# Kernel tuning notes

Hardware: AMD Instinct MI355X
Metric: run time of the kernel (lower is better)

## Reference

```python
import jax, jax.numpy as jnp
import numpy as np

N = 512
E = 64          # neigh_dim = spatial_dim + vel_dim
HID = 256
OUT = 32
SPAT = 32
VEL = 32

_OFFDIAG = np.flatnonzero(~np.eye(N, dtype=bool))  # static off-diagonal flat indices


def setup_inputs() -> dict:
    key = jax.random.key(0)
    ks = jax.random.split(key, 24)
    g = lambda i, shape, s=0.05: jax.random.normal(ks[i], shape, dtype=jnp.float32) * s
    return {
        "hidden_state": jax.random.normal(ks[0], (N, HID), dtype=jnp.float32),
        "obs1": jax.random.normal(ks[1], (N, 2), dtype=jnp.float32),
        "obs2": jax.random.normal(ks[2], (N, 2), dtype=jnp.float32),
        "h0": g(3, (N, N, E), 0.1),
        "c0": g(4, (N, N, E), 0.1),
        "W_s": g(5, (SPAT, 2)), "b_s": g(6, (SPAT,)),
        "W_v": g(7, (VEL, 2)), "b_v": g(8, (VEL,)),
        "W_hs": g(9, (E, HID)), "b_hs": g(10, (E,)),
        "W_ih": g(11, (4 * E, E)), "b_ih": g(12, (4 * E,)),
        "W_hh": g(13, (4 * E, E)), "b_hh": g(14, (4 * E,)),
        "Wq": g(15, (E, E)), "Wk": g(16, (E, E)), "Wv": g(17, (E, E)),
        "W_in": g(18, (3 * E, E)), "b_in": g(19, (3 * E,)),
        "W_out": g(20, (E, E)), "b_out": g(21, (E,)),
        "W_o": g(22, (OUT, E)), "b_o": g(23, (OUT,)),
        "track_mask": jnp.ones((N,), dtype=bool),
    }


def _forward(hidden_state, obs1, obs2, h0, c0, W_s, b_s, W_v, b_v, W_hs, b_hs,
             W_ih, b_ih, W_hh, b_hh, Wq, Wk, Wv, W_in, b_in, W_out, b_out, W_o, b_o):
    # pairwise relative positions / velocities, off-diagonal only: [N*(N-1), 2]
    rel_pos = (obs2[None, :, :] - obs2[:, None, :]).reshape(N * N, 2)[_OFFDIAG]
    vel = obs2 - obs1
    rel_vel = (vel[None, :, :] - vel[:, None, :]).reshape(N * N, 2)[_OFFDIAG]

    spat_embed = jax.nn.relu(rel_pos @ W_s.T + b_s)
    vel_embed = jax.nn.relu((rel_vel * 4.0) @ W_v.T + b_v)
    rel_embed = jnp.concatenate([spat_embed, vel_embed], axis=1)  # [M, E]

    # gather off-diagonal LSTM states and run one LSTMCell step
    h = h0.reshape(N * N, E)[_OFFDIAG]
    c = c0.reshape(N * N, E)[_OFFDIAG]
    gates = rel_embed @ W_ih.T + b_ih + h @ W_hh.T + b_hh  # [M, 4E]
    i_g, f_g, g_g, o_g = jnp.split(gates, 4, axis=1)
    c_new = jax.nn.sigmoid(f_g) * c + jax.nn.sigmoid(i_g) * jnp.tanh(g_g)
    h_new = jax.nn.sigmoid(o_g) * jnp.tanh(c_new)  # [M, E]

    hs = hidden_state @ W_hs.T + b_hs  # [N, E]
    # embedded: [N, N, E] -> transpose to (L=N, B=N, E)
    embedded = jnp.concatenate([hs[:, None, :], h_new.reshape(N, N - 1, E)], axis=1)
    embedded = jnp.transpose(embedded, (1, 0, 2))

    q = embedded @ Wq.T
    k = embedded @ Wk.T
    v = embedded @ Wv.T

    # torch MultiheadAttention (1 head) internal projections
    Wq2, Wk2, Wv2 = jnp.split(W_in, 3, axis=0)
    bq2, bk2, bv2 = jnp.split(b_in, 3, axis=0)
    scale = 1.0 / jnp.sqrt(jnp.float32(E))
    q2 = (q @ Wq2.T + bq2) * scale
    k2 = k @ Wk2.T + bk2
    v2 = v @ Wv2.T + bv2
    scores = jnp.einsum('lbe,sbe->bls', q2, k2)      # [B=N, L=N, S=N]
    attn = jax.nn.softmax(scores, axis=-1)
    ctx = jnp.einsum('bls,sbe->lbe', attn, v2)       # [L, B, E]
    attn_out = ctx @ W_out.T + b_out

    attn_vectors = attn_out[0]                        # [N, E]
    return attn_vectors @ W_o.T + b_o                 # [N, OUT]


def reference(hidden_state, obs1, obs2, h0, c0, W_s, b_s, W_v, b_v, W_hs, b_hs,
              W_ih, b_ih, W_hh, b_hh, Wq, Wk, Wv, W_in, b_in, W_out, b_out,
              W_o, b_o, track_mask):
    # track_mask assumed all-True: adj_matrix == off-diagonal mask.
    return _forward(hidden_state, obs1, obs2, h0, c0, W_s, b_s, W_v, b_v,
                    W_hs, b_hs, W_ih, b_ih, W_hh, b_hh, Wq, Wk, Wv,
                    W_in, b_in, W_out, b_out, W_o, b_o)
```

## Files before the change

kernel.cpp:

```cpp
#include <hip/hip_runtime.h>
#include <cstdint>

#define NN 512
#define EE 64
#define HIDD 256
#define OUTD 32
#define L2E 1.4426950408889634f

typedef __bf16 bf16x8 __attribute__((ext_vector_type(8)));
typedef __bf16 bf16x4 __attribute__((ext_vector_type(4)));
typedef float f32x4 __attribute__((ext_vector_type(4)));
typedef float f32x2 __attribute__((ext_vector_type(2)));

__device__ float g_WhsT[HIDD*EE];
__device__ uint4 g_Ag2[4096];
__device__ float g_biasI[256];
__device__ float g_embW[EE*4];
__device__ float g_WqT[EE*EE];
__device__ float g_Wq2T[EE*EE];
__device__ float g_WvT[EE*EE];
__device__ float g_Wv2T[EE*EE];
__device__ float g_WoutT[EE*EE];
__device__ float g_WoT[EE*OUTD];

__device__ __forceinline__ float ex2(float x){ return __builtin_amdgcn_exp2f(x); }
__device__ __forceinline__ float rcp_(float x){ return __builtin_amdgcn_rcpf(x); }

__global__ __launch_bounds__(256) void prepW(
    const float* __restrict__ W_ih, const float* __restrict__ b_ih,
    const float* __restrict__ W_hh, const float* __restrict__ b_hh,
    const float* __restrict__ Wq, const float* __restrict__ Wv,
    const float* __restrict__ W_in, const float* __restrict__ W_hs,
    const float* __restrict__ W_s, const float* __restrict__ b_s,
    const float* __restrict__ W_v, const float* __restrict__ b_v,
    const float* __restrict__ W_out, const float* __restrict__ W_o)
{
    const int blk = blockIdx.x, tid = threadIdx.x;
    if (blk < 8) {
#pragma unroll
        for (int ii = 0; ii < 2; ++ii) {
            int idx = blk*512 + ii*256 + tid;
            int w = idx >> 9, mh = (idx >> 8) & 1, kh = (idx >> 6) & 3, lane = idx & 63;
            int m = lane & 15, qq = m >> 2, gate = m & 3;
            int e = 8*w + 2*qq + mh;
            int o = gate*64 + e;
            int kb = kh*32 + (lane >> 4)*8;
            float sc = (gate == 2) ? (-2.f*L2E) : (-L2E);
            bf16x8 vv;
#pragma unroll
            for (int j = 0; j < 8; ++j) {
                int k = kb + j;
                float raw = (k < 64) ? W_ih[o*64 + k] : W_hh[o*64 + (k - 64)];
                vv[j] = (__bf16)(sc * raw);
            }
            g_Ag2[idx] = __builtin_bit_cast(uint4, vv);
        }
    } else if (blk == 8) {
        {
            int e = tid >> 2, gate = tid & 3, o = gate*64 + e;
            float sc = (gate == 2) ? (-2.f*L2E) : (-L2E);
            g_biasI[tid] = sc * (b_ih[o] + b_hh[o]);
        }
        if (tid < 64) {
            int e = tid;
            if (e < 32) {
                g_embW[e*4+0] = W_s[e*2]; g_embW[e*4+1] = W_s[e*2+1]; g_embW[e*4+2] = b_s[e];
            } else {
                g_embW[e*4+0] = 4.f*W_v[(e-32)*2]; g_embW[e*4+1] = 4.f*W_v[(e-32)*2+1]; g_embW[e*4+2] = b_v[e-32];
            }
            g_embW[e*4+3] = 0.f;
        }
    } else if (blk == 9) {
        __shared__ float T[64][65];
        for (int kt = 0; kt < 4; ++kt) {
            __syncthreads();
#pragma unroll
            for (int i = 0; i < 16; ++i) {
                int row = i*4 + (tid >> 6);
                int col = tid & 63;
                T[col][row] = W_hs[row*256 + kt*64 + col];
            }
            __syncthreads();
#pragma unroll
            for (int i = 0; i < 16; ++i) {
                int krow = i*4 + (tid >> 6);
                int e = tid & 63;
                g_WhsT[(kt*64 + krow)*64 + e] = T[krow][e];
            }
        }
    } else {
        __shared__ float T[64][65];
        auto tr64 = [&](const float* src, float* dst) {
#pragma unroll
            for (int i = 0; i < 16; ++i) {
                int row = i*4 + (tid >> 6), col = tid & 63;
                T[col][row] = src[row*64 + col];
            }
            __syncthreads();
#pragma unroll
            for (int i = 0; i < 16; ++i) {
                int k = i*4 + (tid >> 6), e = tid & 63;
                dst[k*64 + e] = T[k][e];
            }
            __syncthreads();
        };
        if (blk == 10) {
            tr64(Wq, g_WqT);
            tr64(W_in, g_Wq2T);
        } else if (blk == 11) {
            tr64(Wv, g_WvT);
            tr64(W_in + 2*4096, g_Wv2T);
        } else {
            tr64(W_out, g_WoutT);
#pragma unroll
            for (int i = 0; i < 8; ++i) {
                int row = i*4 + (tid >> 6), col = tid & 63;
                T[col][row] = W_o[row*64 + col];
            }
            __syncthreads();
#pragma unroll
            for (int i = 0; i < 8; ++i) {
                int k = i*8 + (tid >> 5), o = tid & 31;
                g_WoT[k*32 + o] = T[k][o];
            }
        }
    }
}

__global__ __launch_bounds__(512, 4) void row_kernel(
    const float* __restrict__ hidden, const float* __restrict__ b_hs,
    const float* __restrict__ obs1, const float* __restrict__ obs2,
    const float* __restrict__ h0, const float* __restrict__ c0,
    const float* __restrict__ W_in, const float* __restrict__ Wk,
    const float* __restrict__ b_in, const float* __restrict__ b_out,
    const float* __restrict__ b_o, float* __restrict__ out)
{
    __shared__ __align__(16) float Hs[3][32*64];
    __shared__ __align__(16) float Cs[3][32*64];
    __shared__ __align__(16) unsigned short Xe[2][32*64];
    __shared__ float spart[2][8][32];
    __shared__ float2 obs1L[NN], obs2L[NN];
    __shared__ float hid[HIDD];
    __shared__ float part[8][64];
    __shared__ float hsL[64], qkL[64];
    __shared__ float vA[64], vB[64];
    __shared__ float ctxE[64];

    const int b = blockIdx.x, tid = threadIdx.x;
    const int w = tid >> 6, l = tid & 63;
    const int q = l >> 4, r = l & 15;
    const int ebase0 = 8*w + 2*q;
    const float* h0r = h0 + (size_t)b*NN*EE;
    const float* c0r = c0 + (size_t)b*NN*EE;

    auto stageT = [&](const float* gsrc, float* lbuf) {
        const int row = tid >> 4;
        const int cb  = (tid & 15) * 16;
        const char* g = (const char*)gsrc + row*256 + (cb ^ ((row & 15) << 4));
        char* lp = (char*)lbuf + tid*16;
        __builtin_amdgcn_global_load_lds(
            (const __attribute__((address_space(1))) void*)g,
            (__attribute__((address_space(3))) void*)lp, 16, 0, 0);
    };

    auto matvecG = [&](const float* M, const float* vin, float* vout,
                       const float* bias, float scale) {
        float s = 0.f;
#pragma unroll
        for (int k2 = 0; k2 < 8; ++k2) {
            int kk = w*8 + k2;
            s = fmaf(M[kk*64 + l], vin[kk], s);
        }
        part[w][l] = s;
        asm volatile("s_waitcnt lgkmcnt(0)" ::: "memory");
        __builtin_amdgcn_s_barrier();
        if (tid < 64) {
            float v = bias ? bias[tid] : 0.f;
#pragma unroll
            for (int i = 0; i < 8; ++i) v += part[i][tid];
            vout[tid] = v * scale;
        }
        asm volatile("s_waitcnt lgkmcnt(0)" ::: "memory");
        __builtin_amdgcn_s_barrier();
    };

    uint4 Afr[2][4];
#pragma unroll
    for (int mh = 0; mh < 2; ++mh)
#pragma unroll
        for (int kh = 0; kh < 4; ++kh)
            Afr[mh][kh] = g_Ag2[w*512 + mh*256 + kh*64 + l];
    f32x4 biasv[2];
#pragma unroll
    for (int mh = 0; mh < 2; ++mh) {
        float4 t4 = *(const float4*)(g_biasI + (ebase0 + mh)*4);
        biasv[mh][0]=t4.x; biasv[mh][1]=t4.y; biasv[mh][2]=t4.z; biasv[mh][3]=t4.w;
    }
    float eA[4], eB[4], eC[4];
    {
        const int e0 = (tid & 15)*4;
#pragma unroll
        for (int i = 0; i < 4; ++i) {
            eA[i] = g_embW[(e0+i)*4+0]; eB[i] = g_embW[(e0+i)*4+1]; eC[i] = g_embW[(e0+i)*4+2];
        }
    }

    const float ob2x = obs2[b*2], ob2y = obs2[b*2+1];
    const float ob1x = obs1[b*2], ob1y = obs1[b*2+1];
    const float velbx = ob2x - ob1x, velby = ob2y - ob1y;
    auto embedW = [&](int jb, unsigned short* xe) {
        const int p = tid >> 4;
        const float2 o2 = obs2L[jb + p];
        const float2 o1 = obs1L[jb + p];
        const float u0s = o2.x - ob2x, u1s = o2.y - ob2y;
        const float u0v = (o2.x - o1.x) - velbx, u1v = (o2.y - o1.y) - velby;
        const bool sph = ((tid & 15) < 8);
        const float u0 = sph ? u0s : u0v, u1 = sph ? u1s : u1v;
        bf16x4 pk;
#pragma unroll
        for (int i = 0; i < 4; ++i)
            pk[i] = (__bf16)fmaxf(fmaf(eA[i], u0, fmaf(eB[i], u1, eC[i])), 0.f);
        *(bf16x4*)((char*)xe + p*128 + (((tid & 15)*8) ^ ((p & 7) << 4))) = pk;
    };

    stageT(h0r, Hs[0]);
    stageT(c0r, Cs[0]);
    stageT(h0r + 32*EE, Hs[1]);
    stageT(c0r + 32*EE, Cs[1]);
    obs2L[tid] = ((const float2*)obs2)[tid];
    obs1L[tid] = ((const float2*)obs1)[tid];
    if (tid < HIDD) hid[tid] = hidden[b*HIDD + tid];
    asm volatile("s_waitcnt lgkmcnt(0)" ::: "memory");
    __builtin_amdgcn_s_barrier();
    __builtin_amdgcn_sched_barrier(0);
    {
        float s = 0.f;
#pragma unroll 8
        for (int k2 = 0; k2 < 32; ++k2) {
            int kk = w*32 + k2;
            s = fmaf(g_WhsT[kk*64 + l], hid[kk], s);
        }
        part[w][l] = s;
    }
    asm volatile("s_waitcnt lgkmcnt(0)" ::: "memory");
    __builtin_amdgcn_s_barrier();
    if (tid < 64) {
        float v = b_hs[tid];
#pragma unroll
        for (int i = 0; i < 8; ++i) v += part[i][tid];
        hsL[tid] = v;
    }
    asm volatile("s_waitcnt lgkmcnt(0)" ::: "memory");
    __builtin_amdgcn_s_barrier();
    matvecG(g_WqT,       hsL, vA, nullptr, 1.f);
    matvecG(g_Wq2T,      vA,  vB, b_in,    1.f);
    matvecG(W_in + 4096, vB,  vA, nullptr, 1.f);
    matvecG(Wk,          vA,  qkL, nullptr, L2E*0.125f);
    embedW(0, Xe[0]);
    const f32x2 qkr = *(const f32x2*)&qkL[ebase0];
    const f32x2 hsd = *(const f32x2*)&hsL[ebase0];
    asm volatile("s_waitcnt vmcnt(2) lgkmcnt(0)" ::: "memory");
    __builtin_amdgcn_s_barrier();
    __builtin_amdgcn_sched_barrier(0);

    float m_run = -__builtin_inff(), l_run = 0.f;
    float ctxa[2] = {0.f, 0.f};
    float Eev[2][2];
    int hb = 0;

#pragma unroll 1
    for (int t = 0; t < 16; ++t) {
        const int base = t*32;
        const int cx = t & 1;

        if (t > 0) {
            const int c = l & 31;
            const float* spp = &spart[cx ^ 1][0][0];
            float s_p = spp[c];
#pragma unroll
            for (int i = 1; i < 8; ++i) s_p += spp[i*32 + c];
            float tm = s_p;
#pragma unroll
            for (int off = 1; off < 32; off <<= 1) tm = fmaxf(tm, __shfl_xor(tm, off, 64));
            float m_new = fmaxf(m_run, tm);
            float corr = ex2(m_run - m_new);
            float wp = ex2(s_p - m_new);
            l_run = fmaf(l_run, corr, wp);
            m_run = m_new;
            float wn0 = __shfl(wp, r, 64);
            float wn1 = __shfl(wp, 16 + r, 64);
#pragma unroll
            for (int mh = 0; mh < 2; ++mh)
                ctxa[mh] = fmaf(wn1, Eev[mh][1], fmaf(wn0, Eev[mh][0], ctxa[mh]*corr));
        }

        const float* HsC = &Hs[hb][0];
        const float* CsC = &Cs[hb][0];
        const unsigned short* XeC = &Xe[cx][0];
        f32x2 cpre[2];
#pragma unroll
        for (int nh = 0; nh < 2; ++nh) {
            const int p = 16*nh + r;
            cpre[nh] = *(const f32x2*)((const char*)CsC + p*256 +
                        ((ebase0*4) ^ ((p & 15) << 4)));
        }
        f32x4 acc[2][2];
#pragma unroll
        for (int mh = 0; mh < 2; ++mh)
#pragma unroll
            for (int nh = 0; nh < 2; ++nh) acc[mh][nh] = biasv[mh];
#pragma unroll
        for (int kh = 0; kh < 4; ++kh) {
            const bf16x8 Af0 = __builtin_bit_cast(bf16x8, Afr[0][kh]);
            const bf16x8 Af1 = __builtin_bit_cast(bf16x8, Afr[1][kh]);
#pragma unroll
            for (int nh = 0; nh < 2; ++nh) {
                const int p = 16*nh + r;
                bf16x8 Bf;
                if (kh < 2) {
                    Bf = *(const bf16x8*)((const char*)XeC + p*128 +
                          ((kh*64 + q*16) ^ ((p & 7) << 4)));
                } else {
                    const char* hbp = (const char*)HsC + p*256;
                    const int cbb = (kh - 2)*128 + q*32;
                    const int sw = (p & 15) << 4;
                    f32x4 f0 = *(const f32x4*)(hbp + (cbb ^ sw));
                    f32x4 f1 = *(const f32x4*)(hbp + ((cbb + 16) ^ sw));
                    Bf[0]=(__bf16)f0[0]; Bf[1]=(__bf16)f0[1]; Bf[2]=(__bf16)f0[2]; Bf[3]=(__bf16)f0[3];
                    Bf[4]=(__bf16)f1[0]; Bf[5]=(__bf16)f1[1]; Bf[6]=(__bf16)f1[2]; Bf[7]=(__bf16)f1[3];
                }
                acc[0][nh] = __builtin_amdgcn_mfma_f32_16x16x32_bf16(Af0, Bf, acc[0][nh], 0, 0, 0);
                acc[1][nh] = __builtin_amdgcn_mfma_f32_16x16x32_bf16(Af1, Bf, acc[1][nh], 0, 0, 0);
            }
        }
        float sp[2] = {0.f, 0.f};
#pragma unroll
        for (int nh = 0; nh < 2; ++nh) {
#pragma unroll
            for (int mh = 0; mh < 2; ++mh) {
                f32x4 g4 = acc[mh][nh];
                float ea = ex2(g4[0]);
                float eg = ex2(g4[2]);
                float itg = (1.f - eg) * rcp_((1.f + ea)*(1.f + eg));
                float sf = rcp_(1.f + ex2(g4[1]));
                float cn = fmaf(sf, cpre[nh][mh], itg);
                float eo = ex2(g4[3]);
                float ec = ex2(-2.f*L2E*cn);
                float h = (1.f - ec) * rcp_((1.f + eo)*(1.f + ec));
                h = (16*nh + r == b - base) ? hsd[mh] : h;
                Eev[mh][nh] = h;
                sp[nh] = fmaf(qkr[mh], h, sp[nh]);
            }
        }
#pragma unroll
        for (int nh = 0; nh < 2; ++nh) {
            float v = sp[nh];
            v += __shfl_xor(v, 16, 64);
            v += __shfl_xor(v, 32, 64);
            if (q == 0) spart[cx][w][16*nh + r] = v;
        }

        if (t < 14) {
            const int hb2 = (hb == 0) ? 2 : hb - 1;
            stageT(h0r + (size_t)(t+2)*32*EE, &Hs[hb2][0]);
            stageT(c0r + (size_t)(t+2)*32*EE, &Cs[hb2][0]);
        }
        if (t < 15) embedW(base + 32, &Xe[cx ^ 1][0]);

        if (t < 14) {
            asm volatile("s_waitcnt vmcnt(2) lgkmcnt(0)" ::: "memory");
        } else {
            asm volatile("s_waitcnt vmcnt(0) lgkmcnt(0)" ::: "memory");
        }
        __builtin_amdgcn_s_barrier();
        __builtin_amdgcn_sched_barrier(0);
        hb = (hb == 2) ? 0 : hb + 1;
    }

    {
        const int c = l & 31;
        const float* spp = &spart[1][0][0];
        float s_p = spp[c];
#pragma unroll
        for (int i = 1; i < 8; ++i) s_p += spp[i*32 + c];
        float tm = s_p;
#pragma unroll
        for (int off = 1; off < 32; off <<= 1) tm = fmaxf(tm, __shfl_xor(tm, off, 64));
        float m_new = fmaxf(m_run, tm);
        float corr = ex2(m_run - m_new);
        float wp = ex2(s_p - m_new);
        l_run = fmaf(l_run, corr, wp);
        m_run = m_new;
        float wn0 = __shfl(wp, r, 64);
        float wn1 = __shfl(wp, 16 + r, 64);
#pragma unroll
        for (int mh = 0; mh < 2; ++mh)
            ctxa[mh] = fmaf(wn1, Eev[mh][1], fmaf(wn0, Eev[mh][0], ctxa[mh]*corr));
    }

    float lred = l_run;
    lred += __shfl_xor(lred, 1, 64); lred += __shfl_xor(lred, 2, 64);
    lred += __shfl_xor(lred, 4, 64); lred += __shfl_xor(lred, 8, 64);
    lred += __shfl_xor(lred, 16, 64);
    const float inv = rcp_(lred);
#pragma unroll
    for (int mh = 0; mh < 2; ++mh) {
        float v = ctxa[mh];
        v += __shfl_xor(v, 1, 64); v += __shfl_xor(v, 2, 64);
        v += __shfl_xor(v, 4, 64); v += __shfl_xor(v, 8, 64);
        if (r == 0) ctxE[ebase0 + mh] = v * inv;
    }
    __syncthreads();
    matvecG(g_WvT,   ctxE, vA, nullptr,    1.f);
    matvecG(g_Wv2T,  vA,   vB, b_in + 128, 1.f);
    matvecG(g_WoutT, vB,   vA, b_out,      1.f);
    {
        if (l < 32) {
            float s = 0.f;
#pragma unroll
            for (int k2 = 0; k2 < 8; ++k2) {
                int kk = w*8 + k2;
                s = fmaf(g_WoT[kk*32 + l], vA[kk], s);
            }
            part[w][l] = s;
        }
        __syncthreads();
        if (tid < 32) {
            float v = b_o[tid];
#pragma unroll
            for (int i = 0; i < 8; ++i) v += part[i][tid];
            out[b*OUTD + tid] = v;
        }
    }
}

extern "C" void kernel_launch(void* const* d_in, const int* in_sizes, int n_in,
                              void* d_out, int out_size, void* d_ws, size_t ws_size,
                              hipStream_t stream) {
    const float* hidden = (const float*)d_in[0];
    const float* obs1   = (const float*)d_in[1];
    const float* obs2   = (const float*)d_in[2];
    const float* h0     = (const float*)d_in[3];
    const float* c0     = (const float*)d_in[4];
    const float* W_s    = (const float*)d_in[5];
    const float* b_s    = (const float*)d_in[6];
    const float* W_v    = (const float*)d_in[7];
    const float* b_v    = (const float*)d_in[8];
    const float* W_hs   = (const float*)d_in[9];
    const float* b_hs   = (const float*)d_in[10];
    const float* W_ih   = (const float*)d_in[11];
    const float* b_ih   = (const float*)d_in[12];
    const float* W_hh   = (const float*)d_in[13];
    const float* b_hh   = (const float*)d_in[14];
    const float* Wq     = (const float*)d_in[15];
    const float* Wk     = (const float*)d_in[16];
    const float* Wv     = (const float*)d_in[17];
    const float* W_in   = (const float*)d_in[18];
    const float* b_in   = (const float*)d_in[19];
    const float* W_out  = (const float*)d_in[20];
    const float* b_out  = (const float*)d_in[21];
    const float* W_o    = (const float*)d_in[22];
    const float* b_o    = (const float*)d_in[23];

    prepW<<<dim3(13), dim3(256), 0, stream>>>(
        W_ih, b_ih, W_hh, b_hh, Wq, Wv, W_in, W_hs, W_s, b_s, W_v, b_v, W_out, W_o);
    row_kernel<<<dim3(NN), dim3(512), 0, stream>>>(
        hidden, b_hs, obs1, obs2, h0, c0, W_in, Wk, b_in, b_out, b_o, (float*)d_out);
}
```

Baseline: 68.26 us.

## Move per-row hs/qk matvec prologue into separate kernel and restructure staging

The per-row hidden-state projection and the query/key matvec chain move out of the main row kernel into a new prepB kernel that writes hs and qk vectors to global memory. The row kernel then starts its h0/c0 async staging right away. It reads obs values directly from global memory with a one-step prefetch instead of staging all of obs into LDS, and issues the next tile's h0/c0 loads at the top of each iteration. It also raises wave priority around the MFMA/LSTM section, which should shorten the serialized prologue and cut LDS use. The cost is an extra kernel launch and a global round trip for hs/qk.

```diff
diff --git a/kernel.cpp b/kernel.cpp
--- a/kernel.cpp
+++ b/kernel.cpp
@@ -7,6 +7,9 @@
 #define OUTD 32
 #define L2E 1.4426950408889634f
 
+#define AS1 __attribute__((address_space(1)))
+#define AS3 __attribute__((address_space(3)))
+
 typedef __bf16 bf16x8 __attribute__((ext_vector_type(8)));
 typedef __bf16 bf16x4 __attribute__((ext_vector_type(4)));
 typedef float f32x4 __attribute__((ext_vector_type(4)));
@@ -16,17 +19,19 @@
 __device__ uint4 g_Ag2[4096];
 __device__ float g_biasI[256];
 __device__ float g_embW[EE*4];
-__device__ float g_WqT[EE*EE];
-__device__ float g_Wq2T[EE*EE];
-__device__ float g_WvT[EE*EE];
-__device__ float g_Wv2T[EE*EE];
-__device__ float g_WoutT[EE*EE];
+__device__ float g_WqT[4096];
+__device__ float g_Wq2T[4096];
+__device__ float g_WvT[4096];
+__device__ float g_Wv2T[4096];
+__device__ float g_WoutT[4096];
 __device__ float g_WoT[EE*OUTD];
+__device__ float g_hs[NN*EE];
+__device__ float g_qk[NN*EE];
 
 __device__ __forceinline__ float ex2(float x){ return __builtin_amdgcn_exp2f(x); }
 __device__ __forceinline__ float rcp_(float x){ return __builtin_amdgcn_rcpf(x); }
 
-__global__ __launch_bounds__(256) void prepW(
+__global__ __launch_bounds__(256) void prepA(
     const float* __restrict__ W_ih, const float* __restrict__ b_ih,
     const float* __restrict__ W_hh, const float* __restrict__ b_hh,
     const float* __restrict__ Wq, const float* __restrict__ Wv,
@@ -35,6 +40,7 @@
     const float* __restrict__ W_v, const float* __restrict__ b_v,
     const float* __restrict__ W_out, const float* __restrict__ W_o)
 {
+    __shared__ float shP[64*65];
     const int blk = blockIdx.x, tid = threadIdx.x;
     if (blk < 8) {
 #pragma unroll
@@ -71,36 +77,32 @@
             g_embW[e*4+3] = 0.f;
         }
     } else if (blk == 9) {
-        __shared__ float T[64][65];
         for (int kt = 0; kt < 4; ++kt) {
             __syncthreads();
 #pragma unroll
             for (int i = 0; i < 16; ++i) {
-                int row = i*4 + (tid >> 6);
-                int col = tid & 63;
-                T[col][row] = W_hs[row*256 + kt*64 + col];
+                int row = i*4 + (tid >> 6), col = tid & 63;
+                shP[col*65 + row] = W_hs[row*256 + kt*64 + col];
             }
             __syncthreads();
 #pragma unroll
             for (int i = 0; i < 16; ++i) {
-                int krow = i*4 + (tid >> 6);
-                int e = tid & 63;
-                g_WhsT[(kt*64 + krow)*64 + e] = T[krow][e];
+                int krow = i*4 + (tid >> 6), e = tid & 63;
+                g_WhsT[(kt*64 + krow)*64 + e] = shP[krow*65 + e];
             }
         }
     } else {
-        __shared__ float T[64][65];
         auto tr64 = [&](const float* src, float* dst) {
 #pragma unroll
             for (int i = 0; i < 16; ++i) {
                 int row = i*4 + (tid >> 6), col = tid & 63;
-                T[col][row] = src[row*64 + col];
+                shP[col*65 + row] = src[row*64 + col];
             }
             __syncthreads();
 #pragma unroll
             for (int i = 0; i < 16; ++i) {
                 int k = i*4 + (tid >> 6), e = tid & 63;
-                dst[k*64 + e] = T[k][e];
+                dst[k*64 + e] = shP[k*65 + e];
             }
             __syncthreads();
         };
@@ -115,23 +117,72 @@
 #pragma unroll
             for (int i = 0; i < 8; ++i) {
                 int row = i*4 + (tid >> 6), col = tid & 63;
-                T[col][row] = W_o[row*64 + col];
+                shP[col*65 + row] = W_o[row*64 + col];
             }
             __syncthreads();
 #pragma unroll
             for (int i = 0; i < 8; ++i) {
                 int k = i*8 + (tid >> 5), o = tid & 31;
-                g_WoT[k*32 + o] = T[k][o];
+                g_WoT[k*32 + o] = shP[k*65 + o];
             }
         }
     }
 }
 
+__global__ __launch_bounds__(256) void prepB(
+    const float* __restrict__ hidden, const float* __restrict__ b_hs,
+    const float* __restrict__ W_in, const float* __restrict__ Wk,
+    const float* __restrict__ b_in)
+{
+    __shared__ float hid[HIDD];
+    __shared__ float part4[4][64];
+    __shared__ float v0[64], v1[64];
+    const int b = blockIdx.x, tid = threadIdx.x;
+    const int e = tid & 63, kq = tid >> 6;
+    hid[tid] = hidden[b*HIDD + tid];
+    __syncthreads();
+    {
+        float s = 0.f;
+#pragma unroll 8
+        for (int k2 = 0; k2 < 64; ++k2) {
+            int kk = kq*64 + k2;
+            s = fmaf(g_WhsT[kk*64 + e], hid[kk], s);
+        }
+        part4[kq][e] = s;
+    }
+    __syncthreads();
+    if (tid < 64) {
+        float v = part4[0][tid] + part4[1][tid] + part4[2][tid] + part4[3][tid] + b_hs[tid];
+        g_hs[b*64 + tid] = v;
+        v0[tid] = v;
+    }
+    __syncthreads();
+    auto mv = [&](const float* M, const float* vin, float* vout,
+                  const float* bias, float scale) {
+        float s = 0.f;
+#pragma unroll
+        for (int k2 = 0; k2 < 16; ++k2) {
+            int kk = kq*16 + k2;
+            s = fmaf(M[kk*64 + e], vin[kk], s);
+        }
+        part4[kq][e] = s;
+        __syncthreads();
+        if (tid < 64) {
+            float v = bias ? bias[tid] : 0.f;
+            v += part4[0][tid] + part4[1][tid] + part4[2][tid] + part4[3][tid];
+            vout[tid] = v * scale;
+        }
+        __syncthreads();
+    };
+    mv(g_WqT,        v0, v1, nullptr, 1.f);
+    mv(g_Wq2T,       v1, v0, b_in,    1.f);
+    mv(W_in + 4096,  v0, v1, nullptr, 1.f);
+    mv(Wk,           v1, g_qk + b*64, nullptr, L2E*0.125f);
+}
+
 __global__ __launch_bounds__(512, 4) void row_kernel(
-    const float* __restrict__ hidden, const float* __restrict__ b_hs,
     const float* __restrict__ obs1, const float* __restrict__ obs2,
     const float* __restrict__ h0, const float* __restrict__ c0,
-    const float* __restrict__ W_in, const float* __restrict__ Wk,
     const float* __restrict__ b_in, const float* __restrict__ b_out,
     const float* __restrict__ b_o, float* __restrict__ out)
 {
@@ -139,12 +190,8 @@
     __shared__ __align__(16) float Cs[3][32*64];
     __shared__ __align__(16) unsigned short Xe[2][32*64];
     __shared__ float spart[2][8][32];
-    __shared__ float2 obs1L[NN], obs2L[NN];
-    __shared__ float hid[HIDD];
     __shared__ float part[8][64];
-    __shared__ float hsL[64], qkL[64];
-    __shared__ float vA[64], vB[64];
-    __shared__ float ctxE[64];
+    __shared__ float vA[64], vB[64], ctxE[64];
 
     const int b = blockIdx.x, tid = threadIdx.x;
     const int w = tid >> 6, l = tid & 63;
@@ -158,31 +205,15 @@
         const int cb  = (tid & 15) * 16;
         const char* g = (const char*)gsrc + row*256 + (cb ^ ((row & 15) << 4));
         char* lp = (char*)lbuf + tid*16;
-        __builtin_amdgcn_global_load_lds(
-            (const __attribute__((address_space(1))) void*)g,
-            (__attribute__((address_space(3))) void*)lp, 16, 0, 0);
+        __builtin_amdgcn_global_load_lds((const AS1 void*)g, (AS3 void*)lp, 16, 0, 0);
     };
 
-    auto matvecG = [&](const float* M, const float* vin, float* vout,
-                       const float* bias, float scale) {
-        float s = 0.f;
-#pragma unroll
-        for (int k2 = 0; k2 < 8; ++k2) {
-            int kk = w*8 + k2;
-            s = fmaf(M[kk*64 + l], vin[kk], s);
-        }
-        part[w][l] = s;
-        asm volatile("s_waitcnt lgkmcnt(0)" ::: "memory");
-        __builtin_amdgcn_s_barrier();
-        if (tid < 64) {
-            float v = bias ? bias[tid] : 0.f;
-#pragma unroll
-            for (int i = 0; i < 8; ++i) v += part[i][tid];
-            vout[tid] = v * scale;
-        }
-        asm volatile("s_waitcnt lgkmcnt(0)" ::: "memory");
-        __builtin_amdgcn_s_barrier();
-    };
+    float2 o2n = *(const float2*)(obs2 + 2*(tid >> 4));
+    float2 o1n = *(const float2*)(obs1 + 2*(tid >> 4));
+    stageT(h0r, &Hs[0][0]);
+    stageT(c0r, &Cs[0][0]);
+    stageT(h0r + 32*EE, &Hs[1][0]);
+    stageT(c0r + 32*EE, &Cs[1][0]);
 
     uint4 Afr[2][4];
 #pragma unroll
@@ -204,14 +235,14 @@
             eA[i] = g_embW[(e0+i)*4+0]; eB[i] = g_embW[(e0+i)*4+1]; eC[i] = g_embW[(e0+i)*4+2];
         }
     }
-
+    const f32x2 qkr = *(const f32x2*)(g_qk + b*64 + ebase0);
+    const f32x2 hsd = *(const f32x2*)(g_hs + b*64 + ebase0);
     const float ob2x = obs2[b*2], ob2y = obs2[b*2+1];
     const float ob1x = obs1[b*2], ob1y = obs1[b*2+1];
     const float velbx = ob2x - ob1x, velby = ob2y - ob1y;
-    auto embedW = [&](int jb, unsigned short* xe) {
+
+    auto embedW = [&](float2 o2, float2 o1, unsigned short* xe) {
         const int p = tid >> 4;
-        const float2 o2 = obs2L[jb + p];
-        const float2 o1 = obs1L[jb + p];
         const float u0s = o2.x - ob2x, u1s = o2.y - ob2y;
         const float u0v = (o2.x - o1.x) - velbx, u1v = (o2.y - o1.y) - velby;
         const bool sph = ((tid & 15) < 8);
@@ -223,42 +254,7 @@
         *(bf16x4*)((char*)xe + p*128 + (((tid & 15)*8) ^ ((p & 7) << 4))) = pk;
     };
 
-    stageT(h0r, Hs[0]);
-    stageT(c0r, Cs[0]);
-    stageT(h0r + 32*EE, Hs[1]);
-    stageT(c0r + 32*EE, Cs[1]);
-    obs2L[tid] = ((const float2*)obs2)[tid];
-    obs1L[tid] = ((const float2*)obs1)[tid];
-    if (tid < HIDD) hid[tid] = hidden[b*HIDD + tid];
-    asm volatile("s_waitcnt lgkmcnt(0)" ::: "memory");
-    __builtin_amdgcn_s_barrier();
-    __builtin_amdgcn_sched_barrier(0);
-    {
-        float s = 0.f;
-#pragma unroll 8
-        for (int k2 = 0; k2 < 32; ++k2) {
-            int kk = w*32 + k2;
-            s = fmaf(g_WhsT[kk*64 + l], hid[kk], s);
-        }
-        part[w][l] = s;
-    }
-    asm volatile("s_waitcnt lgkmcnt(0)" ::: "memory");
-    __builtin_amdgcn_s_barrier();
-    if (tid < 64) {
-        float v = b_hs[tid];
-#pragma unroll
-        for (int i = 0; i < 8; ++i) v += part[i][tid];
-        hsL[tid] = v;
-    }
-    asm volatile("s_waitcnt lgkmcnt(0)" ::: "memory");
-    __builtin_amdgcn_s_barrier();
-    matvecG(g_WqT,       hsL, vA, nullptr, 1.f);
-    matvecG(g_Wq2T,      vA,  vB, b_in,    1.f);
-    matvecG(W_in + 4096, vB,  vA, nullptr, 1.f);
-    matvecG(Wk,          vA,  qkL, nullptr, L2E*0.125f);
-    embedW(0, Xe[0]);
-    const f32x2 qkr = *(const f32x2*)&qkL[ebase0];
-    const f32x2 hsd = *(const f32x2*)&hsL[ebase0];
+    embedW(o2n, o1n, &Xe[0][0]);
     asm volatile("s_waitcnt vmcnt(2) lgkmcnt(0)" ::: "memory");
     __builtin_amdgcn_s_barrier();
     __builtin_amdgcn_sched_barrier(0);
@@ -272,6 +268,16 @@
     for (int t = 0; t < 16; ++t) {
         const int base = t*32;
         const int cx = t & 1;
+
+        if (t < 15) {
+            o2n = *(const float2*)(obs2 + 2*(base + 32 + (tid >> 4)));
+            o1n = *(const float2*)(obs1 + 2*(base + 32 + (tid >> 4)));
+        }
+        if (t < 14) {
+            const int hb2 = (hb == 0) ? 2 : hb - 1;
+            stageT(h0r + (size_t)(t+2)*32*EE, &Hs[hb2][0]);
+            stageT(c0r + (size_t)(t+2)*32*EE, &Cs[hb2][0]);
+        }
 
         if (t > 0) {
             const int c = l & 31;
@@ -304,6 +310,7 @@
             cpre[nh] = *(const f32x2*)((const char*)CsC + p*256 +
                         ((ebase0*4) ^ ((p & 15) << 4)));
         }
+        __builtin_amdgcn_s_setprio(1);
         f32x4 acc[2][2];
 #pragma unroll
         for (int mh = 0; mh < 2; ++mh)
@@ -352,6 +359,7 @@
                 sp[nh] = fmaf(qkr[mh], h, sp[nh]);
             }
         }
+        __builtin_amdgcn_s_setprio(0);
 #pragma unroll
         for (int nh = 0; nh < 2; ++nh) {
             float v = sp[nh];
@@ -360,12 +368,7 @@
             if (q == 0) spart[cx][w][16*nh + r] = v;
         }
 
-        if (t < 14) {
-            const int hb2 = (hb == 0) ? 2 : hb - 1;
-            stageT(h0r + (size_t)(t+2)*32*EE, &Hs[hb2][0]);
-            stageT(c0r + (size_t)(t+2)*32*EE, &Cs[hb2][0]);
-        }
-        if (t < 15) embedW(base + 32, &Xe[cx ^ 1][0]);
+        if (t < 15) embedW(o2n, o1n, &Xe[cx ^ 1][0]);
 
         if (t < 14) {
             asm volatile("s_waitcnt vmcnt(2) lgkmcnt(0)" ::: "memory");
@@ -411,6 +414,24 @@
         if (r == 0) ctxE[ebase0 + mh] = v * inv;
     }
     __syncthreads();
+    auto matvecG = [&](const float* M, const float* vin, float* vout,
+                       const float* bias, float scale) {
+        float s = 0.f;
+#pragma unroll
+        for (int k2 = 0; k2 < 8; ++k2) {
+            int kk = w*8 + k2;
+            s = fmaf(M[kk*64 + l], vin[kk], s);
+        }
+        part[w][l] = s;
+        __syncthreads();
+        if (tid < 64) {
+            float v = bias ? bias[tid] : 0.f;
+#pragma unroll
+            for (int i = 0; i < 8; ++i) v += part[i][tid];
+            vout[tid] = v * scale;
+        }
+        __syncthreads();
+    };
     matvecG(g_WvT,   ctxE, vA, nullptr,    1.f);
     matvecG(g_Wv2T,  vA,   vB, b_in + 128, 1.f);
     matvecG(g_WoutT, vB,   vA, b_out,      1.f);
@@ -462,8 +483,9 @@
     const float* W_o    = (const float*)d_in[22];
     const float* b_o    = (const float*)d_in[23];
 
-    prepW<<<dim3(13), dim3(256), 0, stream>>>(
+    prepA<<<dim3(13), dim3(256), 0, stream>>>(
         W_ih, b_ih, W_hh, b_hh, Wq, Wv, W_in, W_hs, W_s, b_s, W_v, b_v, W_out, W_o);
+    prepB<<<dim3(NN), dim3(256), 0, stream>>>(hidden, b_hs, W_in, Wk, b_in);
     row_kernel<<<dim3(NN), dim3(512), 0, stream>>>(
-        hidden, b_hs, obs1, obs2, h0, c0, W_in, Wk, b_in, b_out, b_o, (float*)d_out);
+        obs1, obs2, h0, c0, b_in, b_out, b_o, (float*)d_out);
 }
```

Result: slower. 75.69 us (+10.9%).
